# Optimization experiments

Measured on AMD Instinct MI355X. Metric: run time of the kernel, lower is better.

The kernel has to match this reference:

```python
import jax, jax.numpy as jnp
import numpy as np

B = 16384
D = 64
NUM_USERS = 1_000_000
NUM_ITEMS = 100_000
NUM_OCC = 21
NUM_GENRES = 18


def setup_inputs() -> dict:
    key = jax.random.key(0)
    ks = jax.random.split(key, 12)
    user_id = jax.random.randint(ks[0], (B,), 0, NUM_USERS)
    item_id = jax.random.randint(ks[1], (B,), 0, NUM_ITEMS)
    occupation = jax.random.randint(ks[2], (B,), 0, NUM_OCC)
    genre = jax.random.randint(ks[3], (B, NUM_GENRES), 0, 2)
    # guarantee at least one active genre per row (original code assumes nonzero rows)
    genre = genre.at[:, 0].set(1)
    std = 0.01
    user_emb = jax.random.normal(ks[4], (NUM_USERS, D), jnp.float32) * std
    user_b = jax.random.normal(ks[5], (NUM_USERS, 1), jnp.float32) * std
    item_emb = jax.random.normal(ks[6], (NUM_ITEMS, D), jnp.float32) * std
    item_b = jax.random.normal(ks[7], (NUM_ITEMS, 1), jnp.float32) * std
    occ_emb = jax.random.normal(ks[8], (NUM_OCC, D), jnp.float32) * std
    occ_b = jax.random.normal(ks[9], (NUM_OCC, 1), jnp.float32) * std
    genre_emb = jax.random.normal(ks[10], (NUM_GENRES, D), jnp.float32) * std
    genre_b = jax.random.normal(ks[11], (NUM_GENRES, 1), jnp.float32) * std
    return dict(user_id=user_id, item_id=item_id, occupation=occupation, genre=genre,
                user_emb=user_emb, user_b=user_b, item_emb=item_emb, item_b=item_b,
                occ_emb=occ_emb, occ_b=occ_b, genre_emb=genre_emb, genre_b=genre_b)


def _multi_scalar_mean(genre, table):
    # EmbeddingMulti: torch.mean(torch.stack(embeddings)) -> scalar mean over
    # selected rows AND all embedding dims. table: [G, d]
    mask = (genre != 0).astype(table.dtype)            # [B, G]
    d = table.shape[1]
    total = (mask @ table).sum(-1)                     # [B] sum over selected rows and dims
    count = mask.sum(-1) * d                           # [B]
    return total / count                               # [B] scalar per row


def reference(user_id, item_id, occupation, genre,
              user_emb, user_b, item_emb, item_b,
              occ_emb, occ_b, genre_emb, genre_b):
    Q = user_emb[user_id]                              # [B, D]
    bq = user_b[user_id].reshape(-1)                   # [B]
    I = item_emb[item_id]                              # [B, D]
    bi = item_b[item_id].reshape(-1)
    O = occ_emb[occupation]                            # [B, D]
    bo = occ_b[occupation].reshape(-1)
    g = _multi_scalar_mean(genre, genre_emb)           # [B] (broadcast scalar per row)
    bg = _multi_scalar_mean(genre, genre_b)            # [B]
    # (I * G).sum(-1) with G = g broadcast over D  ==  g * I.sum(-1)
    return (Q * I).sum(-1) + (O * Q).sum(-1) + g * I.sum(-1) + bq + bi + bo + bg
```

## Files before the change

### kernel.cpp

```cpp
#include <hip/hip_runtime.h>
#include <hip/hip_bf16.h>

#define D 64
#define NUM_GENRES 18

__global__ void genre_rowsum_kernel(const float* __restrict__ genre_emb,
                                    float* __restrict__ rowsum) {
    int j = threadIdx.x;
    if (j < NUM_GENRES) {
        float s = 0.f;
#pragma unroll
        for (int d = 0; d < D; ++d) s += genre_emb[j * D + d];
        rowsum[j] = s;
    }
}

__global__ __launch_bounds__(256) void mf_kernel(
    const int* __restrict__ user_id, const int* __restrict__ item_id,
    const int* __restrict__ occupation, const int* __restrict__ genre,
    const float* __restrict__ user_emb, const float* __restrict__ user_b,
    const float* __restrict__ item_emb, const float* __restrict__ item_b,
    const float* __restrict__ occ_emb, const float* __restrict__ occ_b,
    const float* __restrict__ genre_b, const float* __restrict__ rowsum,
    float* __restrict__ out, int B) {

    int wave = (int)((blockIdx.x * blockDim.x + threadIdx.x) >> 6);
    int lane = threadIdx.x & 63;
    if (wave >= B) return;
    const int b = wave;

    const int uid = user_id[b];
    const int iid = item_id[b];
    const int oc  = occupation[b];

    const float q = user_emb[(size_t)uid * D + lane];
    const float i = item_emb[(size_t)iid * D + lane];
    const float o = occ_emb[(size_t)oc * D + lane];

    float s1 = q * (i + o);
    float s2 = i;

    float gsum = 0.f, gbias = 0.f, gcnt = 0.f;
    if (lane < NUM_GENRES) {
        if (genre[b * NUM_GENRES + lane] != 0) {
            gsum  = rowsum[lane];
            gbias = genre_b[lane];
            gcnt  = 1.f;
        }
    }

#pragma unroll
    for (int off = 32; off > 0; off >>= 1) {
        s1    += __shfl_xor(s1, off, 64);
        s2    += __shfl_xor(s2, off, 64);
        gsum  += __shfl_xor(gsum, off, 64);
        gbias += __shfl_xor(gbias, off, 64);
        gcnt  += __shfl_xor(gcnt, off, 64);
    }

    if (lane == 0) {
        const float g  = gsum / (gcnt * (float)D);
        const float bg = gbias / gcnt;
        out[b] = s1 + g * s2 + user_b[uid] + item_b[iid] + occ_b[oc] + bg;
    }
}

extern "C" void kernel_launch(void* const* d_in, const int* in_sizes, int n_in,
                              void* d_out, int out_size, void* d_ws, size_t ws_size,
                              hipStream_t stream) {
    const int*   user_id    = (const int*)d_in[0];
    const int*   item_id    = (const int*)d_in[1];
    const int*   occupation = (const int*)d_in[2];
    const int*   genre      = (const int*)d_in[3];
    const float* user_emb   = (const float*)d_in[4];
    const float* user_b     = (const float*)d_in[5];
    const float* item_emb   = (const float*)d_in[6];
    const float* item_b     = (const float*)d_in[7];
    const float* occ_emb    = (const float*)d_in[8];
    const float* occ_b      = (const float*)d_in[9];
    const float* genre_emb  = (const float*)d_in[10];
    const float* genre_b    = (const float*)d_in[11];

    float* out    = (float*)d_out;
    float* rowsum = (float*)d_ws;

    const int B = in_sizes[0];

    genre_rowsum_kernel<<<1, 64, 0, stream>>>(genre_emb, rowsum);

    const int waves_per_block = 256 / 64;
    const int grid = (B + waves_per_block - 1) / waves_per_block;
    mf_kernel<<<grid, 256, 0, stream>>>(user_id, item_id, occupation, genre,
                                        user_emb, user_b, item_emb, item_b,
                                        occ_emb, occ_b, genre_b, rowsum,
                                        out, B);
}
```

Measured before the change: 323.0 us.

## Fuse genre rowsum into main kernel with 16-lane float4 rows

Removes the separate genre rowsum kernel launch and instead accumulates the selected genre embedding rows per batch row inside the main kernel, using a ballot-built genre mask. Each batch row is now handled by 16 lanes loading float4 vectors rather than a full 64-lane wave, so each wave covers four rows and the shuffle reduction is shorter. The trade-off is redundant genre-table reads per row (small and cache-resident) and a per-lane serial loop over the active genres.

```diff
diff --git a/kernel.cpp b/kernel.cpp
--- a/kernel.cpp
+++ b/kernel.cpp
@@ -4,64 +4,82 @@
 #define D 64
 #define NUM_GENRES 18
 
-__global__ void genre_rowsum_kernel(const float* __restrict__ genre_emb,
-                                    float* __restrict__ rowsum) {
-    int j = threadIdx.x;
-    if (j < NUM_GENRES) {
-        float s = 0.f;
-#pragma unroll
-        for (int d = 0; d < D; ++d) s += genre_emb[j * D + d];
-        rowsum[j] = s;
-    }
-}
-
-__global__ __launch_bounds__(256) void mf_kernel(
+__global__ __launch_bounds__(256) void mf_fused(
     const int* __restrict__ user_id, const int* __restrict__ item_id,
     const int* __restrict__ occupation, const int* __restrict__ genre,
     const float* __restrict__ user_emb, const float* __restrict__ user_b,
     const float* __restrict__ item_emb, const float* __restrict__ item_b,
     const float* __restrict__ occ_emb, const float* __restrict__ occ_b,
-    const float* __restrict__ genre_b, const float* __restrict__ rowsum,
+    const float* __restrict__ genre_emb, const float* __restrict__ genre_b,
     float* __restrict__ out, int B) {
 
-    int wave = (int)((blockIdx.x * blockDim.x + threadIdx.x) >> 6);
-    int lane = threadIdx.x & 63;
-    if (wave >= B) return;
-    const int b = wave;
+    const int t   = blockIdx.x * blockDim.x + threadIdx.x;
+    const int row = t >> 4;
+    const int l   = threadIdx.x & 15;
+    const bool active = (row < B);
 
-    const int uid = user_id[b];
-    const int iid = item_id[b];
-    const int oc  = occupation[b];
+    int uid = 0, iid = 0, oc = 0;
+    if (active) {
+        uid = user_id[row];
+        iid = item_id[row];
+        oc  = occupation[row];
+    }
 
-    const float q = user_emb[(size_t)uid * D + lane];
-    const float i = item_emb[(size_t)iid * D + lane];
-    const float o = occ_emb[(size_t)oc * D + lane];
+    int fa = 0, fb = 0;
+    if (active) {
+        fa = genre[row * NUM_GENRES + l];
+        if (l < 2) fb = genre[row * NUM_GENRES + 16 + l];
+    }
+    unsigned long long ba = __ballot(fa != 0);
+    unsigned long long bb = __ballot(fb != 0);
+    const int gsh = (threadIdx.x & 63) & ~15;
+    const unsigned int mask =
+        (unsigned int)((ba >> gsh) & 0xFFFFull) |
+        ((unsigned int)((bb >> gsh) & 0x3ull) << 16);
 
-    float s1 = q * (i + o);
-    float s2 = i;
+    const float4* ue4 = (const float4*)user_emb;
+    const float4* ie4 = (const float4*)item_emb;
+    const float4* oe4 = (const float4*)occ_emb;
+    const float4* ge4 = (const float4*)genre_emb;
 
-    float gsum = 0.f, gbias = 0.f, gcnt = 0.f;
-    if (lane < NUM_GENRES) {
-        if (genre[b * NUM_GENRES + lane] != 0) {
-            gsum  = rowsum[lane];
-            gbias = genre_b[lane];
-            gcnt  = 1.f;
-        }
+    float4 q  = make_float4(0.f, 0.f, 0.f, 0.f);
+    float4 i4 = q, o4 = q;
+    if (active) {
+        q  = ue4[(size_t)uid * 16 + l];
+        i4 = ie4[(size_t)iid * 16 + l];
+        o4 = oe4[(size_t)oc  * 16 + l];
+    }
+
+    float4 gacc = make_float4(0.f, 0.f, 0.f, 0.f);
+    unsigned int m = mask;
+    while (m) {
+        int j = __builtin_ctz(m);
+        m &= m - 1;
+        float4 e = ge4[j * 16 + l];
+        gacc.x += e.x; gacc.y += e.y; gacc.z += e.z; gacc.w += e.w;
+    }
+
+    float s1 = q.x*(i4.x+o4.x) + q.y*(i4.y+o4.y) + q.z*(i4.z+o4.z) + q.w*(i4.w+o4.w);
+    float si = i4.x + i4.y + i4.z + i4.w;
+    float sg = gacc.x + gacc.y + gacc.z + gacc.w;
+    float gb = 0.f;
+    if (active) {
+        if (fa)           gb += genre_b[l];
+        if (l < 2 && fb)  gb += genre_b[16 + l];
     }
 
 #pragma unroll
-    for (int off = 32; off > 0; off >>= 1) {
-        s1    += __shfl_xor(s1, off, 64);
-        s2    += __shfl_xor(s2, off, 64);
-        gsum  += __shfl_xor(gsum, off, 64);
-        gbias += __shfl_xor(gbias, off, 64);
-        gcnt  += __shfl_xor(gcnt, off, 64);
+    for (int off = 8; off > 0; off >>= 1) {
+        s1 += __shfl_xor(s1, off, 64);
+        si += __shfl_xor(si, off, 64);
+        sg += __shfl_xor(sg, off, 64);
+        gb += __shfl_xor(gb, off, 64);
     }
 
-    if (lane == 0) {
-        const float g  = gsum / (gcnt * (float)D);
-        const float bg = gbias / gcnt;
-        out[b] = s1 + g * s2 + user_b[uid] + item_b[iid] + occ_b[oc] + bg;
+    if (active && l == 0) {
+        const float cnt = (float)__builtin_popcount(mask);
+        const float g   = sg / (cnt * (float)D);
+        out[row] = s1 + g * si + user_b[uid] + item_b[iid] + occ_b[oc] + gb / cnt;
     }
 }
 
@@ -81,17 +99,13 @@
     const float* genre_emb  = (const float*)d_in[10];
     const float* genre_b    = (const float*)d_in[11];
 
-    float* out    = (float*)d_out;
-    float* rowsum = (float*)d_ws;
-
+    float* out = (float*)d_out;
     const int B = in_sizes[0];
 
-    genre_rowsum_kernel<<<1, 64, 0, stream>>>(genre_emb, rowsum);
-
-    const int waves_per_block = 256 / 64;
-    const int grid = (B + waves_per_block - 1) / waves_per_block;
-    mf_kernel<<<grid, 256, 0, stream>>>(user_id, item_id, occupation, genre,
-                                        user_emb, user_b, item_emb, item_b,
-                                        occ_emb, occ_b, genre_b, rowsum,
-                                        out, B);
+    const int threads = 256;
+    const int grid = (B * 16 + threads - 1) / threads;
+    mf_fused<<<grid, threads, 0, stream>>>(user_id, item_id, occupation, genre,
+                                           user_emb, user_b, item_emb, item_b,
+                                           occ_emb, occ_b, genre_emb, genre_b,
+                                           out, B);
 }
```

Measured after the change: 320.0 us. Within noise of the previous version (-0.9%).
